# Performance work log

Measured on AMD Instinct MI355X. Metric: run time of the kernel, lower is better.

The kernel has to match this reference:

```python
import jax, jax.numpy as jnp
import numpy as np

N = 50000          # nodes
E = 800000         # edges (before self loops)
D_IN = 128         # input_dim
HID = 64           # hidden_dim (per head)
HEADS = 2
DM = HID * HEADS   # 128, post-concat dim
OUT = 32           # out_channels
G = 64             # graphs in batch
EPS = 1e-5
SLOPE = 0.2        # GATConv negative_slope default


def setup_inputs() -> dict:
    key = jax.random.key(0)
    ks = jax.random.split(key, 24)
    s = 0.1
    return {
        "x": jax.random.normal(ks[0], (N, D_IN), jnp.float32),
        "edge_index": jax.random.randint(ks[1], (2, E), 0, N, jnp.int32),
        "batch": jnp.sort(jax.random.randint(ks[2], (N,), 0, G, jnp.int32)),
        # GAT layer 1
        "W1": jax.random.normal(ks[3], (D_IN, DM), jnp.float32) * s,
        "att_src1": jax.random.normal(ks[4], (HEADS, HID), jnp.float32) * s,
        "att_dst1": jax.random.normal(ks[5], (HEADS, HID), jnp.float32) * s,
        "b1": jnp.zeros((DM,), jnp.float32),
        "ln1_g": jnp.ones((DM,), jnp.float32),
        "ln1_b": jnp.zeros((DM,), jnp.float32),
        # skip connection
        "Wskip": jax.random.normal(ks[6], (D_IN, DM), jnp.float32) * s,
        "bskip": jnp.zeros((DM,), jnp.float32),
        # GAT layer 2
        "W2": jax.random.normal(ks[7], (DM, DM), jnp.float32) * s,
        "att_src2": jax.random.normal(ks[8], (HEADS, HID), jnp.float32) * s,
        "att_dst2": jax.random.normal(ks[9], (HEADS, HID), jnp.float32) * s,
        "b2": jnp.zeros((DM,), jnp.float32),
        "ln2_g": jnp.ones((DM,), jnp.float32),
        "ln2_b": jnp.zeros((DM,), jnp.float32),
        # head
        "Wfc": jax.random.normal(ks[10], (DM, OUT), jnp.float32) * s,
        "bfc": jnp.zeros((OUT,), jnp.float32),
        "bn_g": jnp.ones((OUT,), jnp.float32),
        "bn_b": jnp.zeros((OUT,), jnp.float32),
    }


def _layer_norm(x, g, b):
    m = x.mean(-1, keepdims=True)
    v = ((x - m) ** 2).mean(-1, keepdims=True)
    return (x - m) * jax.lax.rsqrt(v + EPS) * g + b


def _gat(h_in, W, att_src, att_dst, bias, src, dst):
    # PyG GATConv (concat=True): h = x W reshaped to [N,H,C]
    h = (h_in @ W).reshape(N, HEADS, HID)
    a_src = (h * att_src).sum(-1)   # [N,H]
    a_dst = (h * att_dst).sum(-1)   # [N,H]
    e = jax.nn.leaky_relu(a_src[src] + a_dst[dst], SLOPE)  # [E',H]
    # segment softmax over edges sharing target node
    e = e - jax.ops.segment_max(e, dst, num_segments=N)[dst]
    ee = jnp.exp(e)
    denom = jax.ops.segment_sum(ee, dst, num_segments=N)[dst]
    alpha = ee / denom
    msg = h[src] * alpha[:, :, None]               # [E',H,C]
    out = jax.ops.segment_sum(msg, dst, num_segments=N)  # [N,H,C]
    return out.reshape(N, DM) + bias


def reference(x, edge_index, batch, W1, att_src1, att_dst1, b1, ln1_g, ln1_b,
              Wskip, bskip, W2, att_src2, att_dst2, b2, ln2_g, ln2_b,
              Wfc, bfc, bn_g, bn_b):
    # add self loops (PyG GATConv default)
    loop = jnp.arange(N, dtype=edge_index.dtype)
    src = jnp.concatenate([edge_index[0], loop])
    dst = jnp.concatenate([edge_index[1], loop])

    x1 = _gat(x, W1, att_src1, att_dst1, b1, src, dst)
    x1 = jax.nn.elu(_layer_norm(x1, ln1_g, ln1_b))
    x1 = x1 + (x @ Wskip + bskip)          # dropout = identity (eval)

    x2 = _gat(x1, W2, att_src2, att_dst2, b2, src, dst)
    x2 = _layer_norm(x2 + x1, ln2_g, ln2_b)
    emb = jax.nn.elu(x2)

    # global mean pool per graph
    sums = jax.ops.segment_sum(emb, batch, num_segments=G)
    cnt = jax.ops.segment_sum(jnp.ones((N,), emb.dtype), batch, num_segments=G)
    graph_emb = sums / jnp.maximum(cnt, 1.0)[:, None]

    logits = graph_emb @ Wfc + bfc
    # BatchNorm1d (training-mode batch stats, biased var)
    m = logits.mean(0)
    v = ((logits - m) ** 2).mean(0)
    return (logits - m) * jax.lax.rsqrt(v + EPS) * bn_g + bn_b
```

## Files before the change

kernel.cpp:

```cpp
#include <hip/hip_runtime.h>

#define DM    128
#define NHEAD 2
#define HIDC  64
#define OUTC  32
#define NG    64
#define EPS   1e-5f
#define DCAP  64

typedef __attribute__((ext_vector_type(8))) short bf16x8;
typedef __attribute__((ext_vector_type(4))) float f32x4;

__device__ __forceinline__ unsigned short f2bf(float f) {
    union { float f; unsigned int u; } v; v.f = f;
    unsigned int r = v.u + 0x7fffu + ((v.u >> 16) & 1u);
    return (unsigned short)(r >> 16);
}
__device__ __forceinline__ float bflo(unsigned int u) {
    union { unsigned int u; float f; } v; v.u = u << 16; return v.f;
}
__device__ __forceinline__ float bfhi(unsigned int u) {
    union { unsigned int u; float f; } v; v.u = u & 0xffff0000u; return v.f;
}

__global__ __launch_bounds__(256) void prep_kernel(
    const float* __restrict__ W1, const float* __restrict__ Wskip,
    const float* __restrict__ W2,
    unsigned short* __restrict__ wf1, unsigned short* __restrict__ wfs,
    unsigned short* __restrict__ wf2,
    const float* __restrict__ x, unsigned short* __restrict__ xbf, int total,
    int xb, int* __restrict__ cursor, int N,
    float* __restrict__ sums, int sums_n, int cz)
{
    const int b = blockIdx.x;
    if (b < 24) {
        const float* W = b < 8 ? W1 : (b < 16 ? Wskip : W2);
        unsigned short* WF = b < 8 ? wf1 : (b < 16 ? wfs : wf2);
        const int idx = (b & 7) * 256 + threadIdx.x;
        const int nt   = idx >> 8;
        const int ks   = (idx >> 6) & 3;
        const int lane = idx & 63;
        const int c    = nt * 16 + (lane & 15);
        const int k0   = ks * 32 + (lane >> 4) * 8;
        bf16x8 f;
#pragma unroll
        for (int j = 0; j < 8; ++j)
            f[j] = (short)f2bf(W[(k0 + j) * DM + c]);
        ((bf16x8*)WF)[idx] = f;
    } else if (b < 24 + xb) {
        const int i = ((b - 24) * 256 + threadIdx.x) * 4;
        if (i < total) {
            const float4 v = *(const float4*)&x[i];
            ushort4 o;
            o.x = f2bf(v.x); o.y = f2bf(v.y); o.z = f2bf(v.z); o.w = f2bf(v.w);
            *(ushort4*)&xbf[i] = o;
        }
    } else if (b < 24 + xb + cz) {
        const int i0 = ((b - 24 - xb) * 256 + threadIdx.x) * 4;
#pragma unroll
        for (int k = 0; k < 4; ++k)
            if (i0 + k < N) cursor[i0 + k] = 0;
    } else {
        const int i0 = ((b - 24 - xb - cz) * 256 + threadIdx.x) * 4;
#pragma unroll
        for (int k = 0; k < 4; ++k)
            if (i0 + k < sums_n) sums[i0 + k] = 0.f;
    }
}

__device__ __forceinline__ void gemm_body(
    const unsigned short* __restrict__ Xbf, int N,
    const unsigned short* __restrict__ Wfrag,
    const float* __restrict__ bias,
    const float* __restrict__ att_src,
    const float* __restrict__ att_dst,
    unsigned short* __restrict__ Cbf,
    float* __restrict__ a_src,
    float* __restrict__ a_dst,
    int bid, int nblocks)
{
    const int lane = threadIdx.x & 63;
    const int wave = threadIdx.x >> 6;
    const int col  = lane & 15;
    const int kgrp = lane >> 4;

    bf16x8 bfrag[8][4];
    {
        const bf16x8* wf = (const bf16x8*)Wfrag;
#pragma unroll
        for (int nt = 0; nt < 8; ++nt)
#pragma unroll
            for (int ks = 0; ks < 4; ++ks)
                bfrag[nt][ks] = wf[(nt * 4 + ks) * 64 + lane];
    }

    float bcol[8];
#pragma unroll
    for (int nt = 0; nt < 8; ++nt)
        bcol[nt] = bias ? bias[nt * 16 + col] : 0.f;

    float as_c[8], ad_c[8];
    if (att_src) {
#pragma unroll
        for (int nt = 0; nt < 8; ++nt) {
            as_c[nt] = att_src[nt * 16 + col];
            ad_c[nt] = att_dst[nt * 16 + col];
        }
    }

    const int ntiles = (N + 15) >> 4;
    for (int tile = bid * 4 + wave; tile < ntiles; tile += nblocks * 4) {
        const int row0 = tile * 16;

        f32x4 acc[8];
#pragma unroll
        for (int nt = 0; nt < 8; ++nt) acc[nt] = (f32x4){0.f, 0.f, 0.f, 0.f};

        const int r = min(row0 + col, N - 1);
#pragma unroll
        for (int ks = 0; ks < 4; ++ks) {
            const int k0 = ks * 32 + kgrp * 8;
            const bf16x8 af = *(const bf16x8*)&Xbf[(size_t)r * DM + k0];
#pragma unroll
            for (int nt = 0; nt < 8; ++nt)
                acc[nt] = __builtin_amdgcn_mfma_f32_16x16x32_bf16(
                              af, bfrag[nt][ks], acc[nt], 0, 0, 0);
        }

        float dots[4][2], dotd[4][2];
        if (att_src) {
#pragma unroll
            for (int reg = 0; reg < 4; ++reg) {
                dots[reg][0] = dots[reg][1] = 0.f;
                dotd[reg][0] = dotd[reg][1] = 0.f;
            }
        }
#pragma unroll
        for (int reg = 0; reg < 4; ++reg) {
            const int row = row0 + kgrp * 4 + reg;
            const bool ok = row < N;
#pragma unroll
            for (int nt = 0; nt < 8; ++nt) {
                const float o = acc[nt][reg] + bcol[nt];
                if (ok) Cbf[(size_t)row * DM + nt * 16 + col] = f2bf(o);
                if (att_src) {
                    dots[reg][nt >> 2] += o * as_c[nt];
                    dotd[reg][nt >> 2] += o * ad_c[nt];
                }
            }
        }
        if (att_src) {
#pragma unroll
            for (int reg = 0; reg < 4; ++reg) {
#pragma unroll
                for (int h = 0; h < 2; ++h) {
                    float vs = dots[reg][h], vd = dotd[reg][h];
#pragma unroll
                    for (int off = 8; off; off >>= 1) {
                        vs += __shfl_xor(vs, off);
                        vd += __shfl_xor(vd, off);
                    }
                    const int row = row0 + kgrp * 4 + reg;
                    if (col == 0 && row < N) {
                        a_src[row * NHEAD + h] = vs;
                        a_dst[row * NHEAD + h] = vd;
                    }
                }
            }
        }
    }
}

__global__ __launch_bounds__(256) void gemm_scatter_kernel(
    const unsigned short* __restrict__ Xbf, int N,
    const unsigned short* __restrict__ wf1,
    const unsigned short* __restrict__ wfs,
    const float* __restrict__ bskip,
    const float* __restrict__ as1, const float* __restrict__ ad1,
    unsigned short* __restrict__ Hbuf, unsigned short* __restrict__ Skipbf,
    float* __restrict__ a_src, float* __restrict__ a_dst,
    const int* __restrict__ ei, int E,
    int* __restrict__ cursor, unsigned short* __restrict__ col)
{
    const int b = blockIdx.x;
    if (b < 256) {
        gemm_body(Xbf, N, wf1, nullptr, as1, ad1, Hbuf, a_src, a_dst, b, 256);
    } else if (b < 512) {
        gemm_body(Xbf, N, wfs, bskip, nullptr, nullptr, Skipbf,
                  nullptr, nullptr, b - 256, 256);
    } else {
        const int e = (b - 512) * 256 + threadIdx.x;
        if (e < E) {
            const int d = ei[E + e];
            const int k = atomicAdd(&cursor[d], 1);
            if (k < DCAP) col[d * DCAP + k] = (unsigned short)ei[e];
        }
    }
}

__global__ __launch_bounds__(256) void mfma_gemm_kernel(
    const unsigned short* __restrict__ Xbf, int N,
    const unsigned short* __restrict__ Wfrag,
    const float* __restrict__ att_src,
    const float* __restrict__ att_dst,
    unsigned short* __restrict__ Cbf,
    float* __restrict__ a_src,
    float* __restrict__ a_dst)
{
    gemm_body(Xbf, N, Wfrag, nullptr, att_src, att_dst, Cbf,
              a_src, a_dst, blockIdx.x, gridDim.x);
}

__global__ __launch_bounds__(128) void gat_agg_ln_kernel(
    const int* __restrict__ deg,
    const unsigned short* __restrict__ col,
    const unsigned short* __restrict__ H,
    const float* __restrict__ a_src,
    const float* __restrict__ a_dst,
    const float* __restrict__ bias,
    const unsigned short* __restrict__ res,
    const float* __restrict__ lng,
    const float* __restrict__ lnb,
    const unsigned short* __restrict__ skip,
    unsigned short* __restrict__ obf,
    int N)
{
    const int wid  = threadIdx.x >> 6;
    const int d    = blockIdx.x * 2 + wid;
    if (d >= N) return;
    const int lane = threadIdx.x & 63;
    const int half = lane >> 5;
    const int c2   = lane * 2;

    const float ad_h = a_dst[d * NHEAD + half];

    float e0 = a_src[d * NHEAD + half] + ad_h;
    e0 = e0 > 0.f ? e0 : 0.2f * e0;
    const float wself = __expf(e0);
    float den = wself;
    float2 acc;
    {
        const unsigned int hu = *(const unsigned int*)&H[(size_t)d * DM + c2];
        acc.x = wself * bflo(hu);
        acc.y = wself * bfhi(hu);
    }

    const int dg = min(deg[d], DCAP);
    const int p0 = d * DCAP;
    for (int base = 0; base < dg; base += 32) {
        const int m = min(32, dg - base);
        const int el = lane & 31;

        float we = 0.f;
        int s = 0;
        if (el < m) {
            s = (int)col[p0 + base + el];
            float a = a_src[s * NHEAD + half] + ad_h;
            a = a > 0.f ? a : 0.2f * a;
            we = __expf(a);
        }
        float ws = we;
#pragma unroll
        for (int off = 1; off < 32; off <<= 1) ws += __shfl_xor(ws, off);
        den += ws;

        const int hsel = lane & 32;
        int e = 0;
        for (; e + 4 <= m; e += 4) {
            const int s0 = __shfl(s, e),     s1 = __shfl(s, e + 1);
            const int s2 = __shfl(s, e + 2), s3 = __shfl(s, e + 3);
            const float w0 = __shfl(we, hsel | e),       w1 = __shfl(we, hsel | (e + 1));
            const float w2 = __shfl(we, hsel | (e + 2)), w3 = __shfl(we, hsel | (e + 3));
            const unsigned int u0 = *(const unsigned int*)&H[(size_t)s0 * DM + c2];
            const unsigned int u1 = *(const unsigned int*)&H[(size_t)s1 * DM + c2];
            const unsigned int u2 = *(const unsigned int*)&H[(size_t)s2 * DM + c2];
            const unsigned int u3 = *(const unsigned int*)&H[(size_t)s3 * DM + c2];
            acc.x += w0 * bflo(u0) + w1 * bflo(u1) + w2 * bflo(u2) + w3 * bflo(u3);
            acc.y += w0 * bfhi(u0) + w1 * bfhi(u1) + w2 * bfhi(u2) + w3 * bfhi(u3);
        }
        for (; e < m; ++e) {
            const int sE = __shfl(s, e);
            const float wE = __shfl(we, hsel | e);
            const unsigned int uE = *(const unsigned int*)&H[(size_t)sE * DM + c2];
            acc.x += wE * bflo(uE);
            acc.y += wE * bfhi(uE);
        }
    }

    const size_t ibase = (size_t)d * DM + c2;
    const float2 bv = *(const float2*)&bias[c2];
    float vx = acc.x / den + bv.x;
    float vy = acc.y / den + bv.y;
    if (res) {
        const unsigned int ru = *(const unsigned int*)&res[ibase];
        vx += bflo(ru); vy += bfhi(ru);
    }

    float sm = vx + vy;
#pragma unroll
    for (int off = 1; off < 64; off <<= 1) sm += __shfl_xor(sm, off);
    const float mean = sm * (1.f / DM);

    const float dx = vx - mean, dy = vy - mean;
    float s2 = dx * dx + dy * dy;
#pragma unroll
    for (int off = 1; off < 64; off <<= 1) s2 += __shfl_xor(s2, off);
    const float rstd = rsqrtf(s2 * (1.f / DM) + EPS);

    const float2 gv = *(const float2*)&lng[c2];
    const float2 bb = *(const float2*)&lnb[c2];
    float yx = dx * rstd * gv.x + bb.x;
    float yy = dy * rstd * gv.y + bb.y;
    yx = yx > 0.f ? yx : expm1f(yx);
    yy = yy > 0.f ? yy : expm1f(yy);
    if (skip) {
        const unsigned int su = *(const unsigned int*)&skip[ibase];
        yx += bflo(su); yy += bfhi(su);
    }
    const unsigned int pk = (unsigned int)f2bf(yx) |
                            ((unsigned int)f2bf(yy) << 16);
    *(unsigned int*)&obf[ibase] = pk;
}

__global__ void pool_kernel(const unsigned short* __restrict__ emb,
                            const int* __restrict__ batch, int N,
                            float* __restrict__ sums,
                            float* __restrict__ cnt)
{
    const int t = threadIdx.x;
    const int chunk = (N + gridDim.x - 1) / gridDim.x;
    const int n0 = blockIdx.x * chunk;
    const int n1 = min(N, n0 + chunk);
    if (n0 >= n1) return;

    int cur = batch[n0];
    float acc = 0.f;
    int count = 0;
    for (int n = n0; n < n1; ++n) {
        int b = batch[n];
        if (b != cur) {
            atomicAdd(&sums[cur * DM + t], acc);
            if (t == 0) atomicAdd(&cnt[cur], (float)count);
            acc = 0.f; count = 0; cur = b;
        }
        unsigned short h = emb[(size_t)n * DM + t];
        union { unsigned int u; float f; } v; v.u = ((unsigned int)h) << 16;
        acc += v.f;
        ++count;
    }
    atomicAdd(&sums[cur * DM + t], acc);
    if (t == 0) atomicAdd(&cnt[cur], (float)count);
}

__global__ void head_kernel(const float* __restrict__ sums,
                            const float* __restrict__ cnt,
                            const float* __restrict__ Wfc,
                            const float* __restrict__ bfc,
                            const float* __restrict__ bn_g,
                            const float* __restrict__ bn_b,
                            float* __restrict__ out)
{
    __shared__ float ge[NG * DM];
    __shared__ float lg[NG * OUTC];
    __shared__ float mu[OUTC], inv[OUTC];
    const int t = threadIdx.x;

    for (int i = t; i < NG * DM; i += blockDim.x) {
        int g = i >> 7;
        ge[i] = sums[i] / fmaxf(cnt[g], 1.0f);
    }
    __syncthreads();

    for (int i = t; i < NG * OUTC; i += blockDim.x) {
        int g = i >> 5, o = i & (OUTC - 1);
        float acc = bfc[o];
#pragma unroll
        for (int k = 0; k < DM; ++k) acc += ge[g * DM + k] * Wfc[k * OUTC + o];
        lg[i] = acc;
    }
    __syncthreads();

    if (t < OUTC) {
        float s = 0.f;
        for (int g = 0; g < NG; ++g) s += lg[g * OUTC + t];
        float m = s * (1.f / NG);
        float v = 0.f;
        for (int g = 0; g < NG; ++g) { float d = lg[g * OUTC + t] - m; v += d * d; }
        v *= (1.f / NG);
        mu[t] = m;
        inv[t] = rsqrtf(v + EPS) * bn_g[t];
    }
    __syncthreads();

    for (int i = t; i < NG * OUTC; i += blockDim.x) {
        int o = i & (OUTC - 1);
        out[i] = (lg[i] - mu[o]) * inv[o] + bn_b[o];
    }
}

extern "C" void kernel_launch(void* const* d_in, const int* in_sizes, int n_in,
                              void* d_out, int out_size, void* d_ws, size_t ws_size,
                              hipStream_t stream)
{
    const float* x     = (const float*)d_in[0];
    const int*   ei    = (const int*)  d_in[1];
    const int*   batch = (const int*)  d_in[2];
    const float* W1    = (const float*)d_in[3];
    const float* as1   = (const float*)d_in[4];
    const float* ad1   = (const float*)d_in[5];
    const float* b1    = (const float*)d_in[6];
    const float* ln1g  = (const float*)d_in[7];
    const float* ln1b  = (const float*)d_in[8];
    const float* Wskip = (const float*)d_in[9];
    const float* bskip = (const float*)d_in[10];
    const float* W2    = (const float*)d_in[11];
    const float* as2   = (const float*)d_in[12];
    const float* ad2   = (const float*)d_in[13];
    const float* b2    = (const float*)d_in[14];
    const float* ln2g  = (const float*)d_in[15];
    const float* ln2b  = (const float*)d_in[16];
    const float* Wfc   = (const float*)d_in[17];
    const float* bfc   = (const float*)d_in[18];
    const float* bng   = (const float*)d_in[19];
    const float* bnb   = (const float*)d_in[20];

    const int N  = in_sizes[2];
    const int E  = in_sizes[1] / 2;

    size_t off = 0;
    auto alloc = [&](size_t bytes) -> char* {
        char* p = (char*)d_ws + off;
        off += (bytes + 255) & ~(size_t)255;
        return p;
    };
    unsigned short* Hbuf   = (unsigned short*)alloc((size_t)N * DM * 2);
    unsigned short* xbf    = (unsigned short*)alloc((size_t)N * DM * 2);
    unsigned short* Buf1bf = (unsigned short*)alloc((size_t)N * DM * 2);
    unsigned short* Buf2bf = (unsigned short*)alloc((size_t)N * DM * 2);
    unsigned short* Skipbf = (unsigned short*)alloc((size_t)N * DM * 2);
    float* asrc   = (float*)alloc((size_t)N * NHEAD * 4);
    float* adst   = (float*)alloc((size_t)N * NHEAD * 4);
    int*   cursor = (int*)  alloc((size_t)N * 4);
    unsigned short* col = (unsigned short*)alloc((size_t)N * DCAP * 2);
    unsigned short* wf1 = (unsigned short*)alloc((size_t)2048 * 8 * 2);
    unsigned short* wfs = (unsigned short*)alloc((size_t)2048 * 8 * 2);
    unsigned short* wf2 = (unsigned short*)alloc((size_t)2048 * 8 * 2);
    float* sums   = (float*)alloc((size_t)(NG * DM + NG) * 4);
    float* cnt    = sums + NG * DM;

    const int eb = (E + 255) / 256;
    const int ab = (N + 1) / 2;
    const int xb = (N * DM / 4 + 255) / 256;
    const int cz = (N + 1023) / 1024;
    const int sums_n = NG * DM + NG;
    const int sz = (sums_n + 1023) / 1024;

    prep_kernel<<<24 + xb + cz + sz, 256, 0, stream>>>(
        W1, Wskip, W2, wf1, wfs, wf2, x, xbf, N * DM, xb,
        cursor, N, sums, sums_n, cz);

    gemm_scatter_kernel<<<512 + eb, 256, 0, stream>>>(
        xbf, N, wf1, wfs, bskip, as1, ad1, Hbuf, Skipbf, asrc, adst,
        ei, E, cursor, col);

    gat_agg_ln_kernel<<<ab, 128, 0, stream>>>(cursor, col, Hbuf, asrc, adst,
                                              b1, nullptr, ln1g, ln1b, Skipbf,
                                              Buf1bf, N);

    mfma_gemm_kernel<<<256, 256, 0, stream>>>(Buf1bf, N, wf2, as2, ad2,
                                              Hbuf, asrc, adst);
    gat_agg_ln_kernel<<<ab, 128, 0, stream>>>(cursor, col, Hbuf, asrc, adst,
                                              b2, Buf1bf, ln2g, ln2b, nullptr,
                                              Buf2bf, N);

    pool_kernel<<<1024, DM, 0, stream>>>(Buf2bf, batch, N, sums, cnt);
    head_kernel<<<1, 1024, 0, stream>>>(sums, cnt, Wfc, bfc, bng, bnb, (float*)d_out);
}
```

Measured before the change: 205.5 us.

## Split GAT aggregation into column-sliced gather kernel and separate layernorm kernel

The fused aggregate+layernorm kernel is split in two. A new aggregation kernel gives each block one 16-column slice and 8 nodes; each wave handles 8 edges at once across 8-lane groups and reduces with cross-lane shuffles. It writes fp32 pre-norm values to a new buffer, which a separate kernel then normalises. This aims to increase memory-level parallelism for the neighbour gathers and to keep the H column slice cache-resident across blocks. In exchange it recomputes attention weights 8 times per edge, adds an fp32 intermediate round-trip (N*128*4 bytes written and read twice), and adds two extra launches.

Result: slower. 434.7 us (+111.5%).

```diff
diff --git a/kernel.cpp b/kernel.cpp
--- a/kernel.cpp
+++ b/kernel.cpp
@@ -211,13 +211,72 @@
               a_src, a_dst, blockIdx.x, gridDim.x);
 }
 
-__global__ __launch_bounds__(128) void gat_agg_ln_kernel(
+__global__ __launch_bounds__(256) void agg_slice_kernel(
     const int* __restrict__ deg,
     const unsigned short* __restrict__ col,
     const unsigned short* __restrict__ H,
     const float* __restrict__ a_src,
     const float* __restrict__ a_dst,
     const float* __restrict__ bias,
+    float* __restrict__ vbuf,
+    int N)
+{
+    const int cs   = blockIdx.x & 7;
+    const int j    = blockIdx.x >> 3;
+    const int w    = threadIdx.x >> 6;
+    const int lane = threadIdx.x & 63;
+    const int ei8  = lane >> 3;
+    const int cl   = lane & 7;
+    const int head = cs >> 2;
+    const int cbase = cs * 16 + cl * 2;
+
+#pragma unroll
+    for (int k = 0; k < 2; ++k) {
+        const int d = j * 8 + w * 2 + k;
+        if (d >= N) break;
+
+        const float ad_h = a_dst[d * NHEAD + head];
+        float e0 = a_src[d * NHEAD + head] + ad_h;
+        e0 = e0 > 0.f ? e0 : 0.2f * e0;
+        const float wself = __expf(e0);
+
+        float den_p = 0.f, ax = 0.f, ay = 0.f;
+        const int dg = min(deg[d], DCAP);
+        const int p0 = d * DCAP;
+        for (int base = 0; base < dg; base += 8) {
+            float we = 0.f;
+            unsigned int u = 0;
+            const int ee = base + ei8;
+            if (ee < dg) {
+                const int s = (int)col[p0 + ee];
+                float a = a_src[s * NHEAD + head] + ad_h;
+                a = a > 0.f ? a : 0.2f * a;
+                we = __expf(a);
+                u = *(const unsigned int*)&H[(size_t)s * DM + cbase];
+            }
+            den_p += we;
+            ax += we * bflo(u);
+            ay += we * bfhi(u);
+        }
+#pragma unroll
+        for (int off = 8; off < 64; off <<= 1) {
+            den_p += __shfl_xor(den_p, off);
+            ax    += __shfl_xor(ax, off);
+            ay    += __shfl_xor(ay, off);
+        }
+        if (ei8 == 0) {
+            const unsigned int hu = *(const unsigned int*)&H[(size_t)d * DM + cbase];
+            const float den = den_p + wself;
+            const float rden = 1.f / den;
+            const float vx = (ax + wself * bflo(hu)) * rden + bias[cbase];
+            const float vy = (ay + wself * bfhi(hu)) * rden + bias[cbase + 1];
+            *(float2*)&vbuf[(size_t)d * DM + cbase] = make_float2(vx, vy);
+        }
+    }
+}
+
+__global__ __launch_bounds__(128) void ln_kernel(
+    const float* __restrict__ v,
     const unsigned short* __restrict__ res,
     const float* __restrict__ lng,
     const float* __restrict__ lnb,
@@ -229,79 +288,21 @@
     const int d    = blockIdx.x * 2 + wid;
     if (d >= N) return;
     const int lane = threadIdx.x & 63;
-    const int half = lane >> 5;
     const int c2   = lane * 2;
-
-    const float ad_h = a_dst[d * NHEAD + half];
-
-    float e0 = a_src[d * NHEAD + half] + ad_h;
-    e0 = e0 > 0.f ? e0 : 0.2f * e0;
-    const float wself = __expf(e0);
-    float den = wself;
-    float2 acc;
-    {
-        const unsigned int hu = *(const unsigned int*)&H[(size_t)d * DM + c2];
-        acc.x = wself * bflo(hu);
-        acc.y = wself * bfhi(hu);
-    }
-
-    const int dg = min(deg[d], DCAP);
-    const int p0 = d * DCAP;
-    for (int base = 0; base < dg; base += 32) {
-        const int m = min(32, dg - base);
-        const int el = lane & 31;
-
-        float we = 0.f;
-        int s = 0;
-        if (el < m) {
-            s = (int)col[p0 + base + el];
-            float a = a_src[s * NHEAD + half] + ad_h;
-            a = a > 0.f ? a : 0.2f * a;
-            we = __expf(a);
-        }
-        float ws = we;
-#pragma unroll
-        for (int off = 1; off < 32; off <<= 1) ws += __shfl_xor(ws, off);
-        den += ws;
-
-        const int hsel = lane & 32;
-        int e = 0;
-        for (; e + 4 <= m; e += 4) {
-            const int s0 = __shfl(s, e),     s1 = __shfl(s, e + 1);
-            const int s2 = __shfl(s, e + 2), s3 = __shfl(s, e + 3);
-            const float w0 = __shfl(we, hsel | e),       w1 = __shfl(we, hsel | (e + 1));
-            const float w2 = __shfl(we, hsel | (e + 2)), w3 = __shfl(we, hsel | (e + 3));
-            const unsigned int u0 = *(const unsigned int*)&H[(size_t)s0 * DM + c2];
-            const unsigned int u1 = *(const unsigned int*)&H[(size_t)s1 * DM + c2];
-            const unsigned int u2 = *(const unsigned int*)&H[(size_t)s2 * DM + c2];
-            const unsigned int u3 = *(const unsigned int*)&H[(size_t)s3 * DM + c2];
-            acc.x += w0 * bflo(u0) + w1 * bflo(u1) + w2 * bflo(u2) + w3 * bflo(u3);
-            acc.y += w0 * bfhi(u0) + w1 * bfhi(u1) + w2 * bfhi(u2) + w3 * bfhi(u3);
-        }
-        for (; e < m; ++e) {
-            const int sE = __shfl(s, e);
-            const float wE = __shfl(we, hsel | e);
-            const unsigned int uE = *(const unsigned int*)&H[(size_t)sE * DM + c2];
-            acc.x += wE * bflo(uE);
-            acc.y += wE * bfhi(uE);
-        }
-    }
-
     const size_t ibase = (size_t)d * DM + c2;
-    const float2 bv = *(const float2*)&bias[c2];
-    float vx = acc.x / den + bv.x;
-    float vy = acc.y / den + bv.y;
+
+    float2 vv = *(const float2*)&v[ibase];
     if (res) {
         const unsigned int ru = *(const unsigned int*)&res[ibase];
-        vx += bflo(ru); vy += bfhi(ru);
-    }
-
-    float sm = vx + vy;
+        vv.x += bflo(ru); vv.y += bfhi(ru);
+    }
+
+    float sm = vv.x + vv.y;
 #pragma unroll
     for (int off = 1; off < 64; off <<= 1) sm += __shfl_xor(sm, off);
     const float mean = sm * (1.f / DM);
 
-    const float dx = vx - mean, dy = vy - mean;
+    const float dx = vv.x - mean, dy = vv.y - mean;
     float s2 = dx * dx + dy * dy;
 #pragma unroll
     for (int off = 1; off < 64; off <<= 1) s2 += __shfl_xor(s2, off);
@@ -438,6 +439,7 @@
     unsigned short* Buf1bf = (unsigned short*)alloc((size_t)N * DM * 2);
     unsigned short* Buf2bf = (unsigned short*)alloc((size_t)N * DM * 2);
     unsigned short* Skipbf = (unsigned short*)alloc((size_t)N * DM * 2);
+    float* vbuf   = (float*)alloc((size_t)N * DM * 4);
     float* asrc   = (float*)alloc((size_t)N * NHEAD * 4);
     float* adst   = (float*)alloc((size_t)N * NHEAD * 4);
     int*   cursor = (int*)  alloc((size_t)N * 4);
@@ -449,7 +451,8 @@
     float* cnt    = sums + NG * DM;
 
     const int eb = (E + 255) / 256;
-    const int ab = (N + 1) / 2;
+    const int lb = (N + 1) / 2;
+    const int ab = ((N + 7) / 8) * 8;
     const int xb = (N * DM / 4 + 255) / 256;
     const int cz = (N + 1023) / 1024;
     const int sums_n = NG * DM + NG;
@@ -463,15 +466,17 @@
         xbf, N, wf1, wfs, bskip, as1, ad1, Hbuf, Skipbf, asrc, adst,
         ei, E, cursor, col);
 
-    gat_agg_ln_kernel<<<ab, 128, 0, stream>>>(cursor, col, Hbuf, asrc, adst,
-                                              b1, nullptr, ln1g, ln1b, Skipbf,
-                                              Buf1bf, N);
+    agg_slice_kernel<<<ab, 256, 0, stream>>>(cursor, col, Hbuf, asrc, adst,
+                                             b1, vbuf, N);
+    ln_kernel<<<lb, 128, 0, stream>>>(vbuf, nullptr, ln1g, ln1b, Skipbf,
+                                      Buf1bf, N);
 
     mfma_gemm_kernel<<<256, 256, 0, stream>>>(Buf1bf, N, wf2, as2, ad2,
                                               Hbuf, asrc, adst);
-    gat_agg_ln_kernel<<<ab, 128, 0, stream>>>(cursor, col, Hbuf, asrc, adst,
-                                              b2, Buf1bf, ln2g, ln2b, nullptr,
-                                              Buf2bf, N);
+    agg_slice_kernel<<<ab, 256, 0, stream>>>(cursor, col, Hbuf, asrc, adst,
+                                             b2, vbuf, N);
+    ln_kernel<<<lb, 128, 0, stream>>>(vbuf, Buf1bf, ln2g, ln2b, nullptr,
+                                      Buf2bf, N);
 
     pool_kernel<<<1024, DM, 0, stream>>>(Buf2bf, batch, N, sums, cnt);
     head_kernel<<<1, 1024, 0, stream>>>(sums, cnt, Wfc, bfc, bng, bnb, (float*)d_out);
```
